# Kernel tuning notes

Measured on AMD Instinct MI355X. Metric: run time of the kernel, lower is better.

Reference implementation:

```python
import jax, jax.numpy as jnp
import numpy as np

DT = 1.0
TAU_MEM_INV = 0.05
V_LEAK = 0.0
V_TH = 1.0
ALPHA = 100.0  # norse SuperSpike surrogate slope


@jax.custom_vjp
def spike_fn(x):
    # heaviside forward, SuperSpike surrogate backward (norse default 'super')
    return (x > 0).astype(x.dtype)

def _spike_fwd(x):
    return spike_fn(x), x

def _spike_bwd(x, g):
    return (g / (ALPHA * jnp.abs(x) + 1.0) ** 2,)

spike_fn.defvjp(_spike_fwd, _spike_bwd)


def setup_inputs() -> dict:
    key = jax.random.key(0)
    ks = jax.random.split(key, 7)
    T, B = 100, 256
    sizes = [784, 64, 64, 10]
    inp = jax.random.normal(ks[0], (T, B, 1, sizes[0]), dtype=jnp.float32)
    out = {"inp": inp}
    for i in range(3):
        fan_in = sizes[i]
        out[f"W{i}"] = jax.random.normal(ks[1 + 2 * i], (sizes[i + 1], fan_in), dtype=jnp.float32) * (1.0 / np.sqrt(fan_in)).astype(np.float32)
        out[f"b{i}"] = jax.random.normal(ks[2 + 2 * i], (sizes[i + 1],), dtype=jnp.float32) * 0.01
    return out


def _snn_forward(inp, Ws, bs):
    x_seq = inp.squeeze(2)  # [T, B, 784]
    B = x_seq.shape[1]
    v0 = tuple(jnp.zeros((B, W.shape[0]), x_seq.dtype) for W in Ws)

    def step(vs, x):
        new_vs = []
        layer_sp = []
        for W, b, v in zip(Ws, bs, vs):
            i_cur = x @ W.T + b                                  # [B, out]
            v = v + DT * TAU_MEM_INV * (V_LEAK - v + i_cur)      # leaky integrate
            z = spike_fn(v - V_TH)                               # fire
            v = v - z * V_TH                                     # reset_subtract
            x = z
            new_vs.append(v)
            layer_sp.append(z.reshape(-1))                       # x.flatten() per layer
        return tuple(new_vs), (x, jnp.concatenate(layer_sp))

    _, (out_spikes, layer_spikes) = jax.lax.scan(step, v0, x_seq)
    # out_spikes: [T, B, 10]; layer_spikes flattened time-major like torch.cat(list)
    return out_spikes, layer_spikes.reshape(-1)


def reference(inp, W0, b0, W1, b1, W2, b2):
    return _snn_forward(inp, (W0, W1, W2), (b0, b1, b2))
```

## Files before the change

kernel.cpp:

```cpp
#include <hip/hip_runtime.h>

#define T_STEPS 100
#define BATCH 256
#define NIN 784
#define N0 64
#define N1 64
#define N2 10
#define CHUNK (BATCH*N0 + BATCH*N1 + BATCH*N2)
#define KPAD 800
#define NCH 25
#define I0ELEMS (25600*64)
#define AROW 40
#define ASPL (32*AROW)
#define AWAVE (3*ASPL)

typedef __attribute__((ext_vector_type(8))) short short8;
typedef __attribute__((ext_vector_type(4))) short short4v;
typedef __attribute__((ext_vector_type(4))) float f32x4;

__device__ inline short bf16_rne(float x) {
  unsigned u = __float_as_uint(x);
  unsigned h = (u + 0x7FFFu + ((u >> 16) & 1u)) >> 16;
  return (short)h;
}
__device__ inline float bf16_val(short h) {
  return __uint_as_float(((unsigned)(unsigned short)h) << 16);
}

__global__ __launch_bounds__(256) void prep_w0_pack(
    const float* __restrict__ W0, short* __restrict__ W0p) {
  int idx = blockIdx.x * 256 + threadIdx.x;
  int e  = idx & 7;
  int r1 = idx >> 3;
  int l  = r1 & 63;
  int r2 = r1 >> 6;
  int ct = r2 & 3;
  int r3 = r2 >> 2;
  int p  = r3 % 3;
  int c  = r3 / 3;
  int k   = c * 32 + (l >> 4) * 8 + e;
  int col = ct * 16 + (l & 15);
  float w = (k < NIN) ? W0[col * NIN + k] : 0.0f;
  short h0 = bf16_rne(w);
  float rr1 = w - bf16_val(h0);
  short h1 = bf16_rne(rr1);
  float rr2 = rr1 - bf16_val(h1);
  short h2 = bf16_rne(rr2);
  W0p[idx] = (p == 0) ? h0 : (p == 1) ? h1 : h2;
}

__global__ __launch_bounds__(256) void gemm0_kernel(
    const float* __restrict__ X, const short* __restrict__ W0p,
    const float* __restrict__ b0, float* __restrict__ I0T) {
  __shared__ __align__(16) char smem[4 * 32 * 68 * 4];
  const int tid = threadIdx.x;
  const int r0  = blockIdx.x * 32;
  const int wid = tid >> 6;
  const int l   = tid & 63;
  const int lr  = l & 15;
  const int lk  = l >> 4;

  short* Aw = (short*)smem + wid * AWAVE;
  float (*red)[32][68] = (float(*)[32][68])smem;

  const int kbeg = wid * 192;
  const int ccnt = (wid < 3) ? 6 : 7;
  const int gbase = kbeg >> 5;

  f32x4 acc[2][4];
#pragma unroll
  for (int rt = 0; rt < 2; ++rt)
#pragma unroll
    for (int ct = 0; ct < 4; ++ct) acc[rt][ct] = f32x4{0.f, 0.f, 0.f, 0.f};

  const short8* wp8 = (const short8*)W0p;
  const float4  z4  = {0.f, 0.f, 0.f, 0.f};

  const int srow0 = l >> 3;
  const int sks   = l & 7;

  auto A_LOAD = [&](int kb, float4 xa[4]) {
#pragma unroll
    for (int i = 0; i < 4; ++i) {
      int row = srow0 + i * 8;
      int k   = kb + sks * 4;
      xa[i] = (k < NIN) ? *(const float4*)(X + (size_t)(r0 + row) * NIN + k) : z4;
    }
  };
  auto A_WRITE = [&](float4 xa[4]) {
#pragma unroll
    for (int i = 0; i < 4; ++i) {
      int row = srow0 + i * 8;
      float xs[4] = {xa[i].x, xa[i].y, xa[i].z, xa[i].w};
      short4v v0, v1, v2;
#pragma unroll
      for (int e = 0; e < 4; ++e) {
        float x  = xs[e];
        short h0 = bf16_rne(x);   float rr1 = x - bf16_val(h0);
        short h1 = bf16_rne(rr1); float rr2 = rr1 - bf16_val(h1);
        v0[e] = h0; v1[e] = h1; v2[e] = bf16_rne(rr2);
      }
      short* base = Aw + row * AROW + sks * 4;
      *(short4v*)(base)            = v0;
      *(short4v*)(base + ASPL)     = v1;
      *(short4v*)(base + 2 * ASPL) = v2;
    }
  };

  {
    float4 xa[4];
    A_LOAD(kbeg, xa);
    A_WRITE(xa);
  }

  for (int c = 0; c < ccnt; ++c) {
    const bool more = (c + 1 < ccnt);
    const int g = gbase + c;

    short8 cb[4][3];
#pragma unroll
    for (int ct = 0; ct < 4; ++ct) {
#pragma unroll
      for (int p = 0; p < 3; ++p)
        cb[ct][p] = wp8[(size_t)(((g * 3 + p) * 4 + ct)) * 64 + l];
    }

    float4 xn[4];
    if (more) A_LOAD(kbeg + (c + 1) * 32, xn);

    short8 af[2][3];
#pragma unroll
    for (int rti = 0; rti < 2; ++rti)
#pragma unroll
      for (int p = 0; p < 3; ++p)
        af[rti][p] = *(const short8*)(Aw + p * ASPL + (rti * 16 + lr) * AROW + lk * 8);

#pragma unroll
    for (int ct = 0; ct < 4; ++ct) {
      {
        f32x4 a = acc[0][ct];
        a = __builtin_amdgcn_mfma_f32_16x16x32_bf16(af[0][2], cb[ct][0], a, 0, 0, 0);
        a = __builtin_amdgcn_mfma_f32_16x16x32_bf16(af[0][0], cb[ct][2], a, 0, 0, 0);
        a = __builtin_amdgcn_mfma_f32_16x16x32_bf16(af[0][1], cb[ct][1], a, 0, 0, 0);
        a = __builtin_amdgcn_mfma_f32_16x16x32_bf16(af[0][1], cb[ct][0], a, 0, 0, 0);
        a = __builtin_amdgcn_mfma_f32_16x16x32_bf16(af[0][0], cb[ct][1], a, 0, 0, 0);
        a = __builtin_amdgcn_mfma_f32_16x16x32_bf16(af[0][0], cb[ct][0], a, 0, 0, 0);
        acc[0][ct] = a;
      }
      {
        f32x4 a = acc[1][ct];
        a = __builtin_amdgcn_mfma_f32_16x16x32_bf16(af[1][2], cb[ct][0], a, 0, 0, 0);
        a = __builtin_amdgcn_mfma_f32_16x16x32_bf16(af[1][0], cb[ct][2], a, 0, 0, 0);
        a = __builtin_amdgcn_mfma_f32_16x16x32_bf16(af[1][1], cb[ct][1], a, 0, 0, 0);
        a = __builtin_amdgcn_mfma_f32_16x16x32_bf16(af[1][1], cb[ct][0], a, 0, 0, 0);
        a = __builtin_amdgcn_mfma_f32_16x16x32_bf16(af[1][0], cb[ct][1], a, 0, 0, 0);
        a = __builtin_amdgcn_mfma_f32_16x16x32_bf16(af[1][0], cb[ct][0], a, 0, 0, 0);
        acc[1][ct] = a;
      }
    }

    if (more) A_WRITE(xn);
  }

  __syncthreads();

#pragma unroll
  for (int rt = 0; rt < 2; ++rt)
#pragma unroll
    for (int ct = 0; ct < 4; ++ct)
#pragma unroll
      for (int r = 0; r < 4; ++r)
        red[wid][rt * 16 + lk * 4 + r][ct * 16 + lr] = acc[rt][ct][r];
  __syncthreads();

  const int t0  = r0 >> 8;
  const int bb0 = r0 & 255;
  for (int idx = tid; idx < 32 * 16; idx += 256) {
    int row = idx >> 4, q = idx & 15;
    float4 v  = *(const float4*)&red[0][row][q * 4];
    float4 u1 = *(const float4*)&red[1][row][q * 4];
    float4 u2 = *(const float4*)&red[2][row][q * 4];
    float4 u3 = *(const float4*)&red[3][row][q * 4];
    v.x += u1.x; v.y += u1.y; v.z += u1.z; v.w += u1.w;
    v.x += u2.x; v.y += u2.y; v.z += u2.z; v.w += u2.w;
    v.x += u3.x; v.y += u3.y; v.z += u3.z; v.w += u3.w;
    float4 bv = ((const float4*)b0)[q];
    v.x += bv.x; v.y += bv.y; v.z += bv.z; v.w += bv.w;
    ((float4*)I0T)[((size_t)(bb0 + row) * T_STEPS + t0) * 16 + q] = v;
  }
}

__global__ __launch_bounds__(256) void fused_kernel(
    const float* __restrict__ I0T,
    const float* __restrict__ W1, const float* __restrict__ b1,
    const float* __restrict__ W2, const float* __restrict__ b2,
    float* __restrict__ out) {
  __shared__ float bufA[112][68];
  __shared__ float sW1t[64][68];
  __shared__ float sW2[N2][68];
  __shared__ float sI2[T_STEPS][N2];

  const int b   = blockIdx.x;
  const int tid = threadIdx.x;
  const int j   = tid & 63;
  const int tq  = tid >> 6;
  float* outSpk = out;
  float* laySpk = out + T_STEPS * BATCH * N2;

  {
    const float4* src = (const float4*)I0T + (size_t)b * (T_STEPS * 16);
    for (int idx = tid; idx < T_STEPS * 16; idx += 256) {
      float4 v = src[idx];
      int t = idx >> 4, j4 = idx & 15;
      *(float4*)&bufA[t][j4 * 4] = v;
    }
  }
  __syncthreads();

  if (tq == 0) {
    float v = 0.0f;
#pragma unroll
    for (int g = 0; g < 4; ++g) {
      float ic[25];
#pragma unroll
      for (int i = 0; i < 25; ++i) ic[i] = bufA[g * 25 + i][j];
#pragma unroll
      for (int i = 0; i < 25; ++i) {
        v = v + 0.05f * ((0.0f - v) + ic[i]);
        float z = (v > 1.0f) ? 1.0f : 0.0f;
        v -= z;
        ic[i] = z;
      }
#pragma unroll
      for (int i = 0; i < 25; ++i) bufA[g * 25 + i][j] = ic[i];
    }
  } else {
    for (int idx = tid - 64; idx < 64 * 16; idx += 192) {
      int i = idx >> 4, jv = idx & 15;
      float4 wv = *(const float4*)(W1 + (size_t)i * 64 + jv * 4);
      sW1t[jv * 4 + 0][i] = wv.x;
      sW1t[jv * 4 + 1][i] = wv.y;
      sW1t[jv * 4 + 2][i] = wv.z;
      sW1t[jv * 4 + 3][i] = wv.w;
    }
    for (int idx = tid - 64; idx < N2 * 16; idx += 192) {
      int o = idx >> 4, jv = idx & 15;
      *(float4*)&sW2[o][jv * 4] = *(const float4*)(W2 + (size_t)o * 64 + jv * 4);
    }
  }
  __syncthreads();

  for (int idx = tid; idx < T_STEPS * 16; idx += 256) {
    int t = idx >> 4, jv = idx & 15;
    *(float4*)(laySpk + (size_t)t * CHUNK + b * 64 + jv * 4) =
        *(const float4*)&bufA[t][jv * 4];
  }

  const int iq = tid & 15;
  const int ts = tid >> 4;
  float g1[4][7];
  {
    float4 bias = *(const float4*)(b1 + iq * 4);
#pragma unroll
    for (int tt = 0; tt < 7; ++tt) {
      g1[0][tt] = bias.x; g1[1][tt] = bias.y; g1[2][tt] = bias.z; g1[3][tt] = bias.w;
    }
#pragma unroll
    for (int jq = 0; jq < 16; ++jq) {
      float4 z4[7];
#pragma unroll
      for (int tt = 0; tt < 7; ++tt)
        z4[tt] = *(const float4*)&bufA[ts * 7 + tt][jq * 4];
      float4 w4[4];
#pragma unroll
      for (int e = 0; e < 4; ++e)
        w4[e] = *(const float4*)&sW1t[jq * 4 + e][iq * 4];
#pragma unroll
      for (int e = 0; e < 4; ++e) {
#pragma unroll
        for (int tt = 0; tt < 7; ++tt) {
          float zv = ((const float*)&z4[tt])[e];
          g1[0][tt] = fmaf(zv, w4[e].x, g1[0][tt]);
          g1[1][tt] = fmaf(zv, w4[e].y, g1[1][tt]);
          g1[2][tt] = fmaf(zv, w4[e].z, g1[2][tt]);
          g1[3][tt] = fmaf(zv, w4[e].w, g1[3][tt]);
        }
      }
    }
  }
  __syncthreads();
#pragma unroll
  for (int tt = 0; tt < 7; ++tt) {
    float4 o = {g1[0][tt], g1[1][tt], g1[2][tt], g1[3][tt]};
    *(float4*)&bufA[ts * 7 + tt][iq * 4] = o;
  }
  __syncthreads();

  if (tq == 0) {
    float v = 0.0f;
#pragma unroll
    for (int g = 0; g < 4; ++g) {
      float ic[25];
#pragma unroll
      for (int i = 0; i < 25; ++i) ic[i] = bufA[g * 25 + i][j];
#pragma unroll
      for (int i = 0; i < 25; ++i) {
        v = v + 0.05f * ((0.0f - v) + ic[i]);
        float z = (v > 1.0f) ? 1.0f : 0.0f;
        v -= z;
        ic[i] = z;
      }
#pragma unroll
      for (int i = 0; i < 25; ++i) bufA[g * 25 + i][j] = ic[i];
    }
  }
  __syncthreads();

  for (int idx = tid; idx < T_STEPS * 16; idx += 256) {
    int t = idx >> 4, jv = idx & 15;
    *(float4*)(laySpk + (size_t)t * CHUNK + BATCH * N0 + b * 64 + jv * 4) =
        *(const float4*)&bufA[t][jv * 4];
  }

  for (int idx = tid; idx < T_STEPS * N2; idx += 256) {
    int t = idx / N2, o = idx % N2;
    float a = b2[o];
#pragma unroll
    for (int jq = 0; jq < 16; ++jq) {
      float4 z = *(const float4*)&bufA[t][jq * 4];
      float4 wv = *(const float4*)&sW2[o][jq * 4];
      a += z.x * wv.x;
      a += z.y * wv.y;
      a += z.z * wv.z;
      a += z.w * wv.w;
    }
    sI2[t][o] = a;
  }
  __syncthreads();

  if (tid < N2) {
    float v = 0.0f;
#pragma unroll
    for (int g = 0; g < 4; ++g) {
      float ic[25];
#pragma unroll
      for (int i = 0; i < 25; ++i) ic[i] = sI2[g * 25 + i][tid];
#pragma unroll
      for (int i = 0; i < 25; ++i) {
        v = v + 0.05f * ((0.0f - v) + ic[i]);
        float z = (v > 1.0f) ? 1.0f : 0.0f;
        v -= z;
        ic[i] = z;
      }
#pragma unroll
      for (int i = 0; i < 25; ++i) sI2[g * 25 + i][tid] = ic[i];
    }
  }
  __syncthreads();

  for (int idx = tid; idx < T_STEPS * N2; idx += 256) {
    int t = idx / N2, o = idx % N2;
    float z = sI2[t][o];
    outSpk[(size_t)t * (BATCH * N2) + b * N2 + o] = z;
    laySpk[(size_t)t * CHUNK + BATCH * (N0 + N1) + b * N2 + o] = z;
  }
}

extern "C" void kernel_launch(void* const* d_in, const int* in_sizes, int n_in,
                              void* d_out, int out_size, void* d_ws, size_t ws_size,
                              hipStream_t stream) {
  const float* inp = (const float*)d_in[0];
  const float* W0  = (const float*)d_in[1];
  const float* b0  = (const float*)d_in[2];
  const float* W1  = (const float*)d_in[3];
  const float* b1  = (const float*)d_in[4];
  const float* W2  = (const float*)d_in[5];
  const float* b2  = (const float*)d_in[6];

  float* I0T = (float*)d_ws;
  short* W0p = (short*)(I0T + I0ELEMS);

  prep_w0_pack<<<dim3(600), dim3(256), 0, stream>>>(W0, W0p);
  gemm0_kernel<<<dim3(800), dim3(256), 0, stream>>>(inp, W0p, b0, I0T);
  fused_kernel<<<dim3(BATCH), dim3(256), 0, stream>>>(I0T, W1, b1, W2, b2,
                                                      (float*)d_out);
}
```

Baseline: 65.25 us.

## Fuse layer-0 GEMM into per-batch SNN kernel, dropping the I0T workspace

Removes the separate gemm0 kernel and its global intermediate buffer. Each per-batch block now computes its own layer-0 input currents with split-bf16 MFMA over all 100 timesteps, reading X directly. The bias-added result goes straight into shared memory. This cuts a launch and the write and re-read of the intermediate. In exchange the GEMM runs on only 256 blocks of 4 waves, with no K-split and no load prefetch, so the input stream may become latency-bound.

```diff
diff --git a/kernel.cpp b/kernel.cpp
--- a/kernel.cpp
+++ b/kernel.cpp
@@ -7,15 +7,8 @@
 #define N1 64
 #define N2 10
 #define CHUNK (BATCH*N0 + BATCH*N1 + BATCH*N2)
-#define KPAD 800
-#define NCH 25
-#define I0ELEMS (25600*64)
-#define AROW 40
-#define ASPL (32*AROW)
-#define AWAVE (3*ASPL)
 
 typedef __attribute__((ext_vector_type(8))) short short8;
-typedef __attribute__((ext_vector_type(4))) short short4v;
 typedef __attribute__((ext_vector_type(4))) float f32x4;
 
 __device__ inline short bf16_rne(float x) {
@@ -49,149 +42,9 @@
   W0p[idx] = (p == 0) ? h0 : (p == 1) ? h1 : h2;
 }
 
-__global__ __launch_bounds__(256) void gemm0_kernel(
+__global__ __launch_bounds__(256) void snn_kernel(
     const float* __restrict__ X, const short* __restrict__ W0p,
-    const float* __restrict__ b0, float* __restrict__ I0T) {
-  __shared__ __align__(16) char smem[4 * 32 * 68 * 4];
-  const int tid = threadIdx.x;
-  const int r0  = blockIdx.x * 32;
-  const int wid = tid >> 6;
-  const int l   = tid & 63;
-  const int lr  = l & 15;
-  const int lk  = l >> 4;
-
-  short* Aw = (short*)smem + wid * AWAVE;
-  float (*red)[32][68] = (float(*)[32][68])smem;
-
-  const int kbeg = wid * 192;
-  const int ccnt = (wid < 3) ? 6 : 7;
-  const int gbase = kbeg >> 5;
-
-  f32x4 acc[2][4];
-#pragma unroll
-  for (int rt = 0; rt < 2; ++rt)
-#pragma unroll
-    for (int ct = 0; ct < 4; ++ct) acc[rt][ct] = f32x4{0.f, 0.f, 0.f, 0.f};
-
-  const short8* wp8 = (const short8*)W0p;
-  const float4  z4  = {0.f, 0.f, 0.f, 0.f};
-
-  const int srow0 = l >> 3;
-  const int sks   = l & 7;
-
-  auto A_LOAD = [&](int kb, float4 xa[4]) {
-#pragma unroll
-    for (int i = 0; i < 4; ++i) {
-      int row = srow0 + i * 8;
-      int k   = kb + sks * 4;
-      xa[i] = (k < NIN) ? *(const float4*)(X + (size_t)(r0 + row) * NIN + k) : z4;
-    }
-  };
-  auto A_WRITE = [&](float4 xa[4]) {
-#pragma unroll
-    for (int i = 0; i < 4; ++i) {
-      int row = srow0 + i * 8;
-      float xs[4] = {xa[i].x, xa[i].y, xa[i].z, xa[i].w};
-      short4v v0, v1, v2;
-#pragma unroll
-      for (int e = 0; e < 4; ++e) {
-        float x  = xs[e];
-        short h0 = bf16_rne(x);   float rr1 = x - bf16_val(h0);
-        short h1 = bf16_rne(rr1); float rr2 = rr1 - bf16_val(h1);
-        v0[e] = h0; v1[e] = h1; v2[e] = bf16_rne(rr2);
-      }
-      short* base = Aw + row * AROW + sks * 4;
-      *(short4v*)(base)            = v0;
-      *(short4v*)(base + ASPL)     = v1;
-      *(short4v*)(base + 2 * ASPL) = v2;
-    }
-  };
-
-  {
-    float4 xa[4];
-    A_LOAD(kbeg, xa);
-    A_WRITE(xa);
-  }
-
-  for (int c = 0; c < ccnt; ++c) {
-    const bool more = (c + 1 < ccnt);
-    const int g = gbase + c;
-
-    short8 cb[4][3];
-#pragma unroll
-    for (int ct = 0; ct < 4; ++ct) {
-#pragma unroll
-      for (int p = 0; p < 3; ++p)
-        cb[ct][p] = wp8[(size_t)(((g * 3 + p) * 4 + ct)) * 64 + l];
-    }
-
-    float4 xn[4];
-    if (more) A_LOAD(kbeg + (c + 1) * 32, xn);
-
-    short8 af[2][3];
-#pragma unroll
-    for (int rti = 0; rti < 2; ++rti)
-#pragma unroll
-      for (int p = 0; p < 3; ++p)
-        af[rti][p] = *(const short8*)(Aw + p * ASPL + (rti * 16 + lr) * AROW + lk * 8);
-
-#pragma unroll
-    for (int ct = 0; ct < 4; ++ct) {
-      {
-        f32x4 a = acc[0][ct];
-        a = __builtin_amdgcn_mfma_f32_16x16x32_bf16(af[0][2], cb[ct][0], a, 0, 0, 0);
-        a = __builtin_amdgcn_mfma_f32_16x16x32_bf16(af[0][0], cb[ct][2], a, 0, 0, 0);
-        a = __builtin_amdgcn_mfma_f32_16x16x32_bf16(af[0][1], cb[ct][1], a, 0, 0, 0);
-        a = __builtin_amdgcn_mfma_f32_16x16x32_bf16(af[0][1], cb[ct][0], a, 0, 0, 0);
-        a = __builtin_amdgcn_mfma_f32_16x16x32_bf16(af[0][0], cb[ct][1], a, 0, 0, 0);
-        a = __builtin_amdgcn_mfma_f32_16x16x32_bf16(af[0][0], cb[ct][0], a, 0, 0, 0);
-        acc[0][ct] = a;
-      }
-      {
-        f32x4 a = acc[1][ct];
-        a = __builtin_amdgcn_mfma_f32_16x16x32_bf16(af[1][2], cb[ct][0], a, 0, 0, 0);
-        a = __builtin_amdgcn_mfma_f32_16x16x32_bf16(af[1][0], cb[ct][2], a, 0, 0, 0);
-        a = __builtin_amdgcn_mfma_f32_16x16x32_bf16(af[1][1], cb[ct][1], a, 0, 0, 0);
-        a = __builtin_amdgcn_mfma_f32_16x16x32_bf16(af[1][1], cb[ct][0], a, 0, 0, 0);
-        a = __builtin_amdgcn_mfma_f32_16x16x32_bf16(af[1][0], cb[ct][1], a, 0, 0, 0);
-        a = __builtin_amdgcn_mfma_f32_16x16x32_bf16(af[1][0], cb[ct][0], a, 0, 0, 0);
-        acc[1][ct] = a;
-      }
-    }
-
-    if (more) A_WRITE(xn);
-  }
-
-  __syncthreads();
-
-#pragma unroll
-  for (int rt = 0; rt < 2; ++rt)
-#pragma unroll
-    for (int ct = 0; ct < 4; ++ct)
-#pragma unroll
-      for (int r = 0; r < 4; ++r)
-        red[wid][rt * 16 + lk * 4 + r][ct * 16 + lr] = acc[rt][ct][r];
-  __syncthreads();
-
-  const int t0  = r0 >> 8;
-  const int bb0 = r0 & 255;
-  for (int idx = tid; idx < 32 * 16; idx += 256) {
-    int row = idx >> 4, q = idx & 15;
-    float4 v  = *(const float4*)&red[0][row][q * 4];
-    float4 u1 = *(const float4*)&red[1][row][q * 4];
-    float4 u2 = *(const float4*)&red[2][row][q * 4];
-    float4 u3 = *(const float4*)&red[3][row][q * 4];
-    v.x += u1.x; v.y += u1.y; v.z += u1.z; v.w += u1.w;
-    v.x += u2.x; v.y += u2.y; v.z += u2.z; v.w += u2.w;
-    v.x += u3.x; v.y += u3.y; v.z += u3.z; v.w += u3.w;
-    float4 bv = ((const float4*)b0)[q];
-    v.x += bv.x; v.y += bv.y; v.z += bv.z; v.w += bv.w;
-    ((float4*)I0T)[((size_t)(bb0 + row) * T_STEPS + t0) * 16 + q] = v;
-  }
-}
-
-__global__ __launch_bounds__(256) void fused_kernel(
-    const float* __restrict__ I0T,
+    const float* __restrict__ b0,
     const float* __restrict__ W1, const float* __restrict__ b1,
     const float* __restrict__ W2, const float* __restrict__ b2,
     float* __restrict__ out) {
@@ -202,17 +55,91 @@
 
   const int b   = blockIdx.x;
   const int tid = threadIdx.x;
+  const int wid = tid >> 6;
+  const int l   = tid & 63;
+  const int lr  = l & 15;
+  const int lk  = l >> 4;
   const int j   = tid & 63;
   const int tq  = tid >> 6;
   float* outSpk = out;
   float* laySpk = out + T_STEPS * BATCH * N2;
 
+  const int tile0 = wid;
+  const int tile1 = wid + 4;
+  const int nt    = (tile1 < 7) ? 2 : 1;
+
+  f32x4 acc[2][4];
+#pragma unroll
+  for (int i = 0; i < 2; ++i)
+#pragma unroll
+    for (int ct = 0; ct < 4; ++ct) acc[i][ct] = f32x4{0.f, 0.f, 0.f, 0.f};
+
+  const short8* wp8 = (const short8*)W0p;
+  const float4  z4  = {0.f, 0.f, 0.f, 0.f};
+  const int t0g = tile0 * 16 + lr;
+  const int t1g = tile1 * 16 + lr;
+
+  for (int c = 0; c < 25; ++c) {
+    const int kb = c * 32;
+    const int k0 = kb + lk * 8;
+    const bool kok = (k0 < NIN);
+
+    short8 cb[4][3];
+#pragma unroll
+    for (int ct = 0; ct < 4; ++ct)
+#pragma unroll
+      for (int p = 0; p < 3; ++p)
+        cb[ct][p] = wp8[(size_t)((c * 3 + p) * 4 + ct) * 64 + l];
+
+    short8 af[2][3];
+#pragma unroll
+    for (int i = 0; i < 2; ++i) {
+      if (i >= nt) break;
+      const int t = (i == 0) ? t0g : t1g;
+      const bool ok = kok && (t < T_STEPS);
+      const float* xp = X + ((size_t)t * BATCH + b) * NIN + k0;
+      float4 xa = ok ? *(const float4*)(xp)     : z4;
+      float4 xb = ok ? *(const float4*)(xp + 4) : z4;
+      float xs[8] = {xa.x, xa.y, xa.z, xa.w, xb.x, xb.y, xb.z, xb.w};
+#pragma unroll
+      for (int e = 0; e < 8; ++e) {
+        float x  = xs[e];
+        short h0 = bf16_rne(x);   float rr1 = x - bf16_val(h0);
+        short h1 = bf16_rne(rr1); float rr2 = rr1 - bf16_val(h1);
+        af[i][0][e] = h0; af[i][1][e] = h1; af[i][2][e] = bf16_rne(rr2);
+      }
+    }
+
+#pragma unroll
+    for (int i = 0; i < 2; ++i) {
+      if (i >= nt) break;
+#pragma unroll
+      for (int ct = 0; ct < 4; ++ct) {
+        f32x4 a = acc[i][ct];
+        a = __builtin_amdgcn_mfma_f32_16x16x32_bf16(af[i][2], cb[ct][0], a, 0, 0, 0);
+        a = __builtin_amdgcn_mfma_f32_16x16x32_bf16(af[i][0], cb[ct][2], a, 0, 0, 0);
+        a = __builtin_amdgcn_mfma_f32_16x16x32_bf16(af[i][1], cb[ct][1], a, 0, 0, 0);
+        a = __builtin_amdgcn_mfma_f32_16x16x32_bf16(af[i][1], cb[ct][0], a, 0, 0, 0);
+        a = __builtin_amdgcn_mfma_f32_16x16x32_bf16(af[i][0], cb[ct][1], a, 0, 0, 0);
+        a = __builtin_amdgcn_mfma_f32_16x16x32_bf16(af[i][0], cb[ct][0], a, 0, 0, 0);
+        acc[i][ct] = a;
+      }
+    }
+  }
+
   {
-    const float4* src = (const float4*)I0T + (size_t)b * (T_STEPS * 16);
-    for (int idx = tid; idx < T_STEPS * 16; idx += 256) {
-      float4 v = src[idx];
-      int t = idx >> 4, j4 = idx & 15;
-      *(float4*)&bufA[t][j4 * 4] = v;
+    float bv[4];
+#pragma unroll
+    for (int ct = 0; ct < 4; ++ct) bv[ct] = b0[ct * 16 + lr];
+#pragma unroll
+    for (int i = 0; i < 2; ++i) {
+      if (i >= nt) break;
+      const int trow = ((i == 0) ? tile0 : tile1) * 16 + lk * 4;
+#pragma unroll
+      for (int ct = 0; ct < 4; ++ct)
+#pragma unroll
+        for (int r = 0; r < 4; ++r)
+          bufA[trow + r][ct * 16 + lr] = acc[i][ct][r] + bv[ct];
     }
   }
   __syncthreads();
@@ -267,10 +194,10 @@
     }
 #pragma unroll
     for (int jq = 0; jq < 16; ++jq) {
-      float4 z4[7];
+      float4 zv4[7];
 #pragma unroll
       for (int tt = 0; tt < 7; ++tt)
-        z4[tt] = *(const float4*)&bufA[ts * 7 + tt][jq * 4];
+        zv4[tt] = *(const float4*)&bufA[ts * 7 + tt][jq * 4];
       float4 w4[4];
 #pragma unroll
       for (int e = 0; e < 4; ++e)
@@ -279,7 +206,7 @@
       for (int e = 0; e < 4; ++e) {
 #pragma unroll
         for (int tt = 0; tt < 7; ++tt) {
-          float zv = ((const float*)&z4[tt])[e];
+          float zv = ((const float*)&zv4[tt])[e];
           g1[0][tt] = fmaf(zv, w4[e].x, g1[0][tt]);
           g1[1][tt] = fmaf(zv, w4[e].y, g1[1][tt]);
           g1[2][tt] = fmaf(zv, w4[e].z, g1[2][tt]);
@@ -377,11 +304,9 @@
   const float* W2  = (const float*)d_in[5];
   const float* b2  = (const float*)d_in[6];
 
-  float* I0T = (float*)d_ws;
-  short* W0p = (short*)(I0T + I0ELEMS);
+  short* W0p = (short*)d_ws;
 
   prep_w0_pack<<<dim3(600), dim3(256), 0, stream>>>(W0, W0p);
-  gemm0_kernel<<<dim3(800), dim3(256), 0, stream>>>(inp, W0p, b0, I0T);
-  fused_kernel<<<dim3(BATCH), dim3(256), 0, stream>>>(I0T, W1, b1, W2, b2,
-                                                      (float*)d_out);
-}
+  snn_kernel<<<dim3(BATCH), dim3(256), 0, stream>>>(inp, W0p, b0, W1, b1,
+                                                    W2, b2, (float*)d_out);
+}
```

Result: slower. 81.83 us (+25.4%).
